# Kernel tuning notes

Hardware: AMD Instinct MI355X
Metric: run time of the kernel (lower is better)

## Reference

```python
import math
import jax, jax.numpy as jnp
import numpy as np

N = 20000
E = 640000
H = 256          # hidden_channels
HEADS = 8
HD = H // HEADS  # head_dim = 32
RBF = 64
CUT = 5.0
EPS = 1e-5


def setup_inputs() -> dict:
    key = jax.random.key(0)
    ks = jax.random.split(key, 24)
    g = lambda k, shape, scale: (jax.random.normal(k, shape, dtype=jnp.float32) * scale)
    inp = {
        "x": jax.random.normal(ks[0], (N, H), dtype=jnp.float32),
        "vec": jax.random.normal(ks[1], (N, 3, H), dtype=jnp.float32),
        "edge_index": jax.random.randint(ks[2], (2, E), 0, N),
        "r_ij": jax.random.uniform(ks[3], (E,), dtype=jnp.float32) * CUT,
        "f_ij": jax.random.normal(ks[4], (E, RBF), dtype=jnp.float32),
        "d_ij": jax.random.normal(ks[5], (E, 3), dtype=jnp.float32),
        # parameters (weights stored as [in, out], applied as x @ W + b)
        "ln_w": jnp.ones((H,), jnp.float32),
        "ln_b": jnp.zeros((H,), jnp.float32),
        "Wq": g(ks[6], (H, H), 1.0 / math.sqrt(H)),
        "bq": jnp.zeros((H,), jnp.float32),
        "Wk": g(ks[7], (H, H), 1.0 / math.sqrt(H)),
        "bk": jnp.zeros((H,), jnp.float32),
        "Wv": g(ks[8], (H, 3 * H), 1.0 / math.sqrt(H)),
        "bv": jnp.zeros((3 * H,), jnp.float32),
        "Wo": g(ks[9], (H, 3 * H), 1.0 / math.sqrt(H)),
        "bo": jnp.zeros((3 * H,), jnp.float32),
        "Wvec": g(ks[10], (H, 3 * H), 1.0 / math.sqrt(H)),  # no bias
        "Wdk": g(ks[11], (RBF, H), 1.0 / math.sqrt(RBF)),
        "bdk": jnp.zeros((H,), jnp.float32),
        "Wdv": g(ks[12], (RBF, 3 * H), 1.0 / math.sqrt(RBF)),
        "bdv": jnp.zeros((3 * H,), jnp.float32),
    }
    return inp


def reference(x, vec, edge_index, r_ij, f_ij, d_ij,
              ln_w, ln_b, Wq, bq, Wk, bk, Wv, bv, Wo, bo,
              Wvec, Wdk, bdk, Wdv, bdv):
    silu = jax.nn.silu
    n = x.shape[0]

    # LayerNorm over hidden dim
    mu = x.mean(-1, keepdims=True)
    var = ((x - mu) ** 2).mean(-1, keepdims=True)
    xn = (x - mu) / jnp.sqrt(var + EPS) * ln_w + ln_b

    q = (xn @ Wq + bq).reshape(n, HEADS, HD)
    k = (xn @ Wk + bk).reshape(n, HEADS, HD)
    v = (xn @ Wv + bv).reshape(n, HEADS, 3 * HD)

    # vec_proj: [N,3,H] @ [H,3H] -> split into three [N,3,H]
    vec1, vec2, vec3 = jnp.split(vec @ Wvec, 3, axis=-1)
    vec_dot = (vec1 * vec2).sum(axis=1)              # [N, H]
    vec_h = vec.reshape(n, 3, HEADS, HD)

    dk = silu(f_ij @ Wdk + bdk).reshape(-1, HEADS, HD)        # [E,h,hd]
    dv = silu(f_ij @ Wdv + bdv).reshape(-1, HEADS, 3 * HD)    # [E,h,3hd]

    src = edge_index[0]  # j (source)
    dst = edge_index[1]  # i (target), aggregation index

    # per-edge attention with cosine cutoff (cutoff_lower = 0)
    attn = (q[dst] * k[src] * dk).sum(-1)                      # [E, h]
    cut = 0.5 * (jnp.cos(r_ij * (math.pi / CUT)) + 1.0)
    cut = cut * (r_ij < CUT).astype(cut.dtype)
    attn = silu(attn) * cut[:, None]

    v_j = v[src] * dv                                          # [E,h,3hd]
    xm, v1m, v2m = jnp.split(v_j, 3, axis=2)                   # each [E,h,hd]
    xm = xm * attn[..., None]                                  # [E,h,hd]
    # [E,3,h,hd]
    vecm = vec_h[src] * v1m[:, None] + v2m[:, None] * d_ij[:, :, None, None]

    x_agg = jax.ops.segment_sum(xm, dst, num_segments=n).reshape(n, H)
    vec_agg = jax.ops.segment_sum(vecm, dst, num_segments=n).reshape(n, 3, H)

    o1, o2, o3 = jnp.split(x_agg @ Wo + bo, 3, axis=1)
    dx = vec_dot * o2 + o3
    dvec = vec3 * o1[:, None] + vec_agg
    return dx, dvec
```

## Files before the change

### kernel.cpp

```cpp
#include <hip/hip_runtime.h>

#define NN 20000
#define EE 640000
#define H 256
#define H3 768

typedef __attribute__((ext_vector_type(8))) short bfrag;
typedef __attribute__((ext_vector_type(4))) float f32x4;
typedef __attribute__((ext_vector_type(2))) unsigned short u16x2;
typedef __attribute__((ext_vector_type(4))) unsigned short u16x4;
typedef unsigned short u16;

__device__ __forceinline__ float silu_f(float x){ return x / (1.f + __expf(-x)); }

__device__ __forceinline__ u16 f2bf(float f){
  union { float fv; unsigned u; } a; a.fv = f;
  unsigned r = a.u + 0x7fffu + ((a.u >> 16) & 1u);
  return (u16)(r >> 16);
}
__device__ __forceinline__ float bf2f(u16 u){
  union { unsigned u32; float f; } a; a.u32 = ((unsigned)u) << 16; return a.f;
}

__global__ __launch_bounds__(256) void ln_kernel(
    const float* __restrict__ x, const float* __restrict__ w,
    const float* __restrict__ b, float* __restrict__ xn)
{
  int n = blockIdx.x, t = threadIdx.x;
  float v = x[(size_t)n*H + t];
  float s1 = v, s2 = v*v;
  #pragma unroll
  for(int o=32;o>0;o>>=1){ s1 += __shfl_down(s1,o,64); s2 += __shfl_down(s2,o,64); }
  __shared__ float r1[4], r2[4];
  if((t&63)==0){ r1[t>>6]=s1; r2[t>>6]=s2; }
  __syncthreads();
  float mu  = (r1[0]+r1[1]+r1[2]+r1[3]) * (1.f/256.f);
  float ex2 = (r2[0]+r2[1]+r2[2]+r2[3]) * (1.f/256.f);
  float inv = rsqrtf(ex2 - mu*mu + 1e-5f);
  xn[(size_t)n*H + t] = (v - mu)*inv*w[t] + b[t];
}

template<int MODE>
__global__ __launch_bounds__(256) void gemm_node(
    const float* __restrict__ A, const float* __restrict__ W, int ldw,
    const float* __restrict__ bias, float* __restrict__ C,
    u16* __restrict__ Ch, long bufstride, int M)
{
  __shared__ float As[16][68];
  __shared__ float Bs[16][64];
  int tid = threadIdx.x;
  int m0 = blockIdx.x * 64;
  int n0 = blockIdx.y * 64;
  int tx = tid & 15, ty = tid >> 4;
  int arow = tid >> 2;
  int ak   = (tid & 3) * 4;
  int brow = tid >> 4;
  int bcol = (tid & 15) * 4;
  bool aval = (m0 + arow) < M;
  const float* Ap = A + (size_t)(m0 + arow) * 256;
  float acc[4][4] = {};
  for(int kb = 0; kb < 256; kb += 16){
    float4 av = make_float4(0.f,0.f,0.f,0.f);
    if(aval) av = *(const float4*)(Ap + kb + ak);
    As[ak+0][arow] = av.x; As[ak+1][arow] = av.y;
    As[ak+2][arow] = av.z; As[ak+3][arow] = av.w;
    *(float4*)&Bs[brow][bcol] = *(const float4*)(W + (size_t)(kb + brow)*ldw + n0 + bcol);
    __syncthreads();
    #pragma unroll
    for(int kk=0;kk<16;kk++){
      float4 a4 = *(const float4*)&As[kk][ty*4];
      float4 b4 = *(const float4*)&Bs[kk][tx*4];
      float aa[4] = {a4.x,a4.y,a4.z,a4.w};
      float bb[4] = {b4.x,b4.y,b4.z,b4.w};
      #pragma unroll
      for(int i=0;i<4;i++)
        #pragma unroll
        for(int j=0;j<4;j++)
          acc[i][j] += aa[i]*bb[j];
    }
    __syncthreads();
  }
  #pragma unroll
  for(int i=0;i<4;i++){
    int row = m0 + ty*4 + i;
    if(row < M){
      int col = n0 + tx*4;
      float o[4];
      #pragma unroll
      for(int j=0;j<4;j++) o[j] = acc[i][j] + (bias ? bias[col+j] : 0.f);
      if(MODE == 0){
        *(float4*)(C + (size_t)row*ldw + col) = make_float4(o[0],o[1],o[2],o[3]);
      } else if(MODE == 1){
        u16x4 h; h[0]=f2bf(o[0]); h[1]=f2bf(o[1]); h[2]=f2bf(o[2]); h[3]=f2bf(o[3]);
        *(u16x4*)(Ch + (size_t)row*ldw + col) = h;
      } else {
        int buf = n0 >> 8;
        int coff = (n0 & 255) + tx*4;
        *(float4*)(C + (size_t)buf*bufstride + (size_t)row*256 + coff)
            = make_float4(o[0],o[1],o[2],o[3]);
      }
    }
  }
}

__global__ __launch_bounds__(256) void vecdot_kernel(
    const float* __restrict__ vp1, const float* __restrict__ vp2, float* __restrict__ vd)
{
  int i = blockIdx.x*256 + threadIdx.x;
  int n = i >> 8, c = i & 255;
  size_t base = (size_t)(3*n)*256 + c;
  float s = 0.f;
  #pragma unroll
  for(int d=0;d<3;d++) s += vp1[base + d*256] * vp2[base + d*256];
  vd[i] = s;
}

__global__ __launch_bounds__(256) void cvt_bf16(
    const float* __restrict__ src, u16* __restrict__ dst, int n4)
{
  int i = blockIdx.x*256 + threadIdx.x;
  if(i < n4){
    float4 v = ((const float4*)src)[i];
    u16x4 o; o[0]=f2bf(v.x); o[1]=f2bf(v.y); o[2]=f2bf(v.z); o[3]=f2bf(v.w);
    ((u16x4*)dst)[i] = o;
  }
}

__global__ __launch_bounds__(256) void hist_kernel(const int* __restrict__ ei, int* __restrict__ deg){
  int e = blockIdx.x*256 + threadIdx.x;
  if(e < EE) atomicAdd(&deg[ei[EE + e]], 1);
}

__global__ __launch_bounds__(1024) void scan_kernel(const int* __restrict__ deg, int* __restrict__ offs){
  __shared__ int ps[1024];
  int t = threadIdx.x;
  int base = t*20;
  int s = 0;
  for(int i=0;i<20;i++){ int idx = base+i; if(idx < NN) s += deg[idx]; }
  ps[t] = s; __syncthreads();
  for(int off=1; off<1024; off<<=1){
    int v = (t>=off) ? ps[t-off] : 0;
    __syncthreads();
    ps[t] += v;
    __syncthreads();
  }
  int run = (t==0) ? 0 : ps[t-1];
  for(int i=0;i<20;i++){
    int idx = base+i;
    if(idx <= NN){
      offs[idx] = run;
      if(idx < NN) run += deg[idx];
    }
  }
}

__global__ __launch_bounds__(256) void scatter_kernel(
    const int* __restrict__ ei, const int* __restrict__ offs,
    int* __restrict__ cursor, int* __restrict__ perm)
{
  int e = blockIdx.x*256 + threadIdx.x;
  if(e >= EE) return;
  int d = ei[EE + e];
  int r = atomicAdd(&cursor[d], 1);
  perm[offs[d] + r] = e;
}

__global__ __launch_bounds__(256) void conv_wdk(const float* __restrict__ Wdk, short* __restrict__ wdkf){
  int idx = blockIdx.x*256 + threadIdx.x;
  int k = idx >> 8, c = idx & 255;
  int g = c >> 6, rem = c & 63, n15 = rem >> 2, p = rem & 3;
  int half = k >> 5, quad = (k >> 3) & 3, j = k & 7;
  wdkf[(g*4+p)*1024 + half*512 + quad*128 + n15*8 + j] = (short)f2bf(Wdk[k*H + c]);
}

__global__ __launch_bounds__(256) void conv_wdv(const float* __restrict__ Wdv, short* __restrict__ wdvf){
  int idx = blockIdx.x*256 + threadIdx.x;
  int k = idx / 768, c = idx % 768;
  int h = c / 96, jj = c % 96;
  int st = jj >> 5, r32 = jj & 31, n15 = r32 >> 1, p = r32 & 1;
  int sub = h*6 + st*2 + p;
  int half = k >> 5, quad = (k >> 3) & 3, j = k & 7;
  wdvf[sub*1024 + half*512 + quad*128 + n15*8 + j] = (short)f2bf(Wdv[k*H3 + c]);
}

__global__ __launch_bounds__(256,3) void edge_kernel(
    const int* __restrict__ ei, const float* __restrict__ rij,
    const float* __restrict__ fij, const float* __restrict__ dij,
    const float* __restrict__ qg, const u16* __restrict__ kh,
    const u16* __restrict__ vh, const u16* __restrict__ vech,
    const short* __restrict__ wdkf, const short* __restrict__ wdvf,
    const float* __restrict__ bdk, const float* __restrict__ bdv,
    const int* __restrict__ offs, const int* __restrict__ perm,
    float* __restrict__ xagg, float* __restrict__ dvec)
{
  __shared__ float accs_x[4][256];
  __shared__ float accs_v[4][768];
  __shared__ float attn_s[4][16][8];
  __shared__ int   esrc_s[4][16];
  __shared__ float ecut_s[4][16];
  __shared__ float emask_s[4][16];
  __shared__ float edij_s[4][3][16];

  int tid  = threadIdx.x;
  int wv   = tid >> 6, lane = tid & 63;
  int ln15 = lane & 15, quad = lane >> 4;
  int n    = blockIdx.x*4 + wv;
  int rs = offs[n], re = offs[n+1];

  #pragma unroll
  for(int i=0;i<4;i++)  accs_x[wv][i*64 + lane] = 0.f;
  #pragma unroll
  for(int i=0;i<12;i++) accs_v[wv][i*64 + lane] = 0.f;

  float qreg[16], bkreg[16];
  #pragma unroll
  for(int g=0; g<4; g++){
    float4 t = *(const float4*)(qg + (size_t)n*H + g*64 + 4*ln15);
    qreg[g*4+0]=t.x; qreg[g*4+1]=t.y; qreg[g*4+2]=t.z; qreg[g*4+3]=t.w;
    float4 u = *(const float4*)(bdk + g*64 + 4*ln15);
    bkreg[g*4+0]=u.x; bkreg[g*4+1]=u.y; bkreg[g*4+2]=u.z; bkreg[g*4+3]=u.w;
  }

  for(int base = rs; base < re; base += 16){
    int idx = base + ln15;
    bool val = idx < re;
    int e = perm[val ? idx : rs];
    if(quad == 0){
      esrc_s[wv][ln15] = ei[e];
      float r = rij[e];
      float cu = 0.5f*(__cosf(r*0.6283185307f)+1.f);
      cu = (r < 5.f) ? cu : 0.f;
      ecut_s[wv][ln15]  = val ? cu : 0.f;
      emask_s[wv][ln15] = val ? 1.f : 0.f;
      edij_s[wv][0][ln15] = dij[e*3+0];
      edij_s[wv][1][ln15] = dij[e*3+1];
      edij_s[wv][2][ln15] = dij[e*3+2];
    }
    bfrag af0, af1;
    {
      const float* fr = fij + (size_t)e*64 + quad*8;
      float4 fa = *(const float4*)fr;
      float4 fb = *(const float4*)(fr+4);
      float4 fc = *(const float4*)(fr+32);
      float4 fd = *(const float4*)(fr+36);
      af0[0]=(short)f2bf(fa.x); af0[1]=(short)f2bf(fa.y); af0[2]=(short)f2bf(fa.z); af0[3]=(short)f2bf(fa.w);
      af0[4]=(short)f2bf(fb.x); af0[5]=(short)f2bf(fb.y); af0[6]=(short)f2bf(fb.z); af0[7]=(short)f2bf(fb.w);
      af1[0]=(short)f2bf(fc.x); af1[1]=(short)f2bf(fc.y); af1[2]=(short)f2bf(fc.z); af1[3]=(short)f2bf(fc.w);
      af1[4]=(short)f2bf(fd.x); af1[5]=(short)f2bf(fd.y); af1[6]=(short)f2bf(fd.z); af1[7]=(short)f2bf(fd.w);
    }
    int sns[4]; float mk[4];
    #pragma unroll
    for(int r=0;r<4;r++){
      int el = quad*4 + r;
      sns[r] = esrc_s[wv][el];
      mk[r]  = emask_s[wv][el];
    }

    u16x4 kr[4][4];
    #pragma unroll
    for(int g=0;g<4;g++)
      #pragma unroll
      for(int r=0;r<4;r++)
        kr[g][r] = *(const u16x4*)(kh + (size_t)sns[r]*H + g*64 + 4*ln15);

    #pragma unroll
    for(int g=0;g<4;g++){
      float lgg[4] = {0.f,0.f,0.f,0.f};
      #pragma unroll
      for(int p=0;p<4;p++){
        const short* wp = wdkf + (g*4+p)*1024 + quad*128 + ln15*8;
        bfrag b0 = *(const bfrag*)wp;
        bfrag b1 = *(const bfrag*)(wp + 512);
        f32x4 acc = {0.f,0.f,0.f,0.f};
        acc = __builtin_amdgcn_mfma_f32_16x16x32_bf16(af0, b0, acc, 0,0,0);
        acc = __builtin_amdgcn_mfma_f32_16x16x32_bf16(af1, b1, acc, 0,0,0);
        float bias = bkreg[g*4+p], qv = qreg[g*4+p];
        #pragma unroll
        for(int r=0;r<4;r++){
          float dk = silu_f(acc[r] + bias);
          lgg[r] += dk * qv * bf2f(kr[g][r][p]);
        }
      }
      #pragma unroll
      for(int r=0;r<4;r++){
        lgg[r] += __shfl_xor(lgg[r],1,64);
        lgg[r] += __shfl_xor(lgg[r],2,64);
        lgg[r] += __shfl_xor(lgg[r],4,64);
      }
      if((ln15 & 7) == 0){
        int hh = 2*g + (ln15 >> 3);
        #pragma unroll
        for(int r=0;r<4;r++){
          int el = quad*4 + r;
          attn_s[wv][el][hh] = silu_f(lgg[r]) * ecut_s[wv][el];
        }
      }
    }

    #pragma unroll 1
    for(int h=0;h<8;h++){
      u16x2 vld[3][4], vcl[3][4];
      #pragma unroll
      for(int st=0;st<3;st++)
        #pragma unroll
        for(int r=0;r<4;r++)
          vld[st][r] = *(const u16x2*)(vh + (size_t)sns[r]*H3 + h*96 + st*32 + 2*ln15);
      #pragma unroll
      for(int d=0;d<3;d++)
        #pragma unroll
        for(int r=0;r<4;r++)
          vcl[d][r] = *(const u16x2*)(vech + (size_t)sns[r]*H3 + d*H + h*32 + 2*ln15);
      float bb[6];
      #pragma unroll
      for(int st=0;st<3;st++){
        float2 b2 = *(const float2*)(bdv + h*96 + st*32 + 2*ln15);
        bb[st*2] = b2.x; bb[st*2+1] = b2.y;
      }
      float at[4];
      #pragma unroll
      for(int r=0;r<4;r++) at[r] = attn_s[wv][quad*4+r][h];

      float v1v[2][4], vjv[2][4];
      float xmt[2] = {0.f, 0.f};
      #pragma unroll
      for(int st=0;st<3;st++){
        #pragma unroll
        for(int p=0;p<2;p++){
          const short* wp = wdvf + (h*6+st*2+p)*1024 + quad*128 + ln15*8;
          bfrag b0 = *(const bfrag*)wp;
          bfrag b1 = *(const bfrag*)(wp + 512);
          f32x4 acc = {0.f,0.f,0.f,0.f};
          acc = __builtin_amdgcn_mfma_f32_16x16x32_bf16(af0, b0, acc, 0,0,0);
          acc = __builtin_amdgcn_mfma_f32_16x16x32_bf16(af1, b1, acc, 0,0,0);
          float bias = bb[st*2+p];
          #pragma unroll
          for(int r=0;r<4;r++){
            float dvv = silu_f(acc[r] + bias) * mk[r];
            float vj = bf2f(vld[st][r][p]) * dvv;
            if(st == 0)      xmt[p]    += vj * at[r];
            else if(st == 1) v1v[p][r]  = vj;
            else             vjv[p][r]  = vj;
          }
        }
      }
      #pragma unroll
      for(int p=0;p<2;p++){
        xmt[p] += __shfl_xor(xmt[p],16,64);
        xmt[p] += __shfl_xor(xmt[p],32,64);
      }
      if(quad == 0){
        accs_x[wv][h*32 + 2*ln15 + 0] += xmt[0];
        accs_x[wv][h*32 + 2*ln15 + 1] += xmt[1];
      }
      #pragma unroll
      for(int d=0;d<3;d++){
        float t0 = 0.f, t1 = 0.f;
        #pragma unroll
        for(int r=0;r<4;r++){
          float dj = edij_s[wv][d][quad*4+r];
          t0 += bf2f(vcl[d][r][0]) * v1v[0][r] + dj * vjv[0][r];
          t1 += bf2f(vcl[d][r][1]) * v1v[1][r] + dj * vjv[1][r];
        }
        t0 += __shfl_xor(t0,16,64); t0 += __shfl_xor(t0,32,64);
        t1 += __shfl_xor(t1,16,64); t1 += __shfl_xor(t1,32,64);
        if(quad == 0){
          accs_v[wv][d*H + h*32 + 2*ln15 + 0] += t0;
          accs_v[wv][d*H + h*32 + 2*ln15 + 1] += t1;
        }
      }
    }
  }

  #pragma unroll
  for(int j=0;j<4;j++)  xagg[(size_t)n*H  + j*64 + lane] = accs_x[wv][j*64 + lane];
  #pragma unroll
  for(int j=0;j<12;j++) dvec[(size_t)n*H3 + j*64 + lane] = accs_v[wv][j*64 + lane];
}

__global__ __launch_bounds__(256) void final_kernel(
    const float* __restrict__ ob, const float* __restrict__ vd,
    const float* __restrict__ vp3, float* __restrict__ out)
{
  int i = blockIdx.x*256 + threadIdx.x;
  int n = i >> 8, c = i & 255;
  float o1 = ob[(size_t)n*H3 + c];
  float o2 = ob[(size_t)n*H3 + 256 + c];
  float o3 = ob[(size_t)n*H3 + 512 + c];
  out[i] = vd[i]*o2 + o3;
  float* dvec = out + (size_t)NN*H;
  #pragma unroll
  for(int d=0;d<3;d++){
    dvec[(size_t)n*H3 + d*H + c] += vp3[(size_t)(3*n+d)*256 + c] * o1;
  }
}

extern "C" void kernel_launch(void* const* d_in, const int* in_sizes, int n_in,
                              void* d_out, int out_size, void* d_ws, size_t ws_size,
                              hipStream_t stream){
  (void)in_sizes; (void)n_in; (void)out_size; (void)ws_size;
  const float* x    = (const float*)d_in[0];
  const float* vec  = (const float*)d_in[1];
  const int*   ei   = (const int*)d_in[2];
  const float* rij  = (const float*)d_in[3];
  const float* fij  = (const float*)d_in[4];
  const float* dij  = (const float*)d_in[5];
  const float* ln_w = (const float*)d_in[6];
  const float* ln_b = (const float*)d_in[7];
  const float* Wq   = (const float*)d_in[8];
  const float* bq   = (const float*)d_in[9];
  const float* Wk   = (const float*)d_in[10];
  const float* bk   = (const float*)d_in[11];
  const float* Wv   = (const float*)d_in[12];
  const float* bv   = (const float*)d_in[13];
  const float* Wo   = (const float*)d_in[14];
  const float* bo   = (const float*)d_in[15];
  const float* Wvec = (const float*)d_in[16];
  const float* Wdk  = (const float*)d_in[17];
  const float* bdk  = (const float*)d_in[18];
  const float* Wdv  = (const float*)d_in[19];
  const float* bdv  = (const float*)d_in[20];
  float* out = (float*)d_out;
  float* ws  = (float*)d_ws;

  float* qb   = ws;
  float* vd   = ws +  5120000;
  float* xagg = ws + 10240000;
  float* vp1  = ws + 15360000;
  float* vp2  = ws + 30720000;
  float* vp3  = ws + 46080000;
  u16*   kh   = (u16*)(ws + 61440000);
  u16*   vh   = (u16*)(ws + 64000000);
  u16*   vech = (u16*)(ws + 71680000);
  int* deg    = (int*)(ws + 79360000);
  int* offs   = deg + 20032;
  int* cursor = offs + 20032;
  int* perm   = cursor + 20032;
  short* wdkf = (short*)(perm + 640000);
  short* wdvf = wdkf + 16384;

  float* xn = vp1;
  float* ob = vp1;
  float* dvec = out + (size_t)NN*H;

  ln_kernel<<<20000, 256, 0, stream>>>(x, ln_w, ln_b, xn);
  gemm_node<0><<<dim3(313,4),  256, 0, stream>>>(xn, Wq, 256, bq, qb, nullptr, 0, 20000);
  gemm_node<1><<<dim3(313,4),  256, 0, stream>>>(xn, Wk, 256, bk, nullptr, kh, 0, 20000);
  gemm_node<1><<<dim3(313,12), 256, 0, stream>>>(xn, Wv, 768, bv, nullptr, vh, 0, 20000);

  hipMemsetAsync(deg,    0, 20000*sizeof(int), stream);
  hipMemsetAsync(cursor, 0, 20000*sizeof(int), stream);
  hist_kernel<<<2500, 256, 0, stream>>>(ei, deg);
  scan_kernel<<<1, 1024, 0, stream>>>(deg, offs);
  scatter_kernel<<<2500, 256, 0, stream>>>(ei, offs, cursor, perm);
  conv_wdk<<<64,  256, 0, stream>>>(Wdk, wdkf);
  conv_wdv<<<192, 256, 0, stream>>>(Wdv, wdvf);
  cvt_bf16<<<15000, 256, 0, stream>>>(vec, vech, 3840000);

  gemm_node<2><<<dim3(938,12), 256, 0, stream>>>(vec, Wvec, 768, nullptr, vp1, nullptr, 15360000L, 60000);
  vecdot_kernel<<<20000, 256, 0, stream>>>(vp1, vp2, vd);

  edge_kernel<<<5000, 256, 0, stream>>>(ei, rij, fij, dij, qb, kh, vh, vech,
                                        wdkf, wdvf, bdk, bdv, offs, perm,
                                        xagg, dvec);

  gemm_node<0><<<dim3(313,12), 256, 0, stream>>>(xagg, Wo, 768, bo, ob, nullptr, 0, 20000);
  final_kernel<<<20000, 256, 0, stream>>>(ob, vd, vp3, out);
}
```

Before: 2.365 ms.

## Replace FP32 SIMT node GEMMs with split-bf16 MFMA GEMMs and fuse vecdot

Moves all node-level GEMMs (Q/K/V, vec projection, output projection) from scalar FP32 tiled loops onto bf16 MFMA instructions. Near-FP32 accuracy is kept by splitting each operand into hi/lo bf16 parts and issuing three MFMAs per tile. Weights are transposed and split once per call, and layernorm, the vec conversion and the edge aggregation now write hi/lo bf16 outputs directly. The vec1·vec2 product is fused into the projection GEMM through LDS, so the vp1/vp2 intermediates are never written to memory. In exchange it uses three MFMAs per tile and extra conversion kernels, and the GEMMs load fragments straight from global memory with no LDS staging.

```diff
diff --git a/kernel.cpp b/kernel.cpp
--- a/kernel.cpp
+++ b/kernel.cpp
@@ -24,7 +24,7 @@
 
 __global__ __launch_bounds__(256) void ln_kernel(
     const float* __restrict__ x, const float* __restrict__ w,
-    const float* __restrict__ b, float* __restrict__ xn)
+    const float* __restrict__ b, u16* __restrict__ xnh, u16* __restrict__ xnl)
 {
   int n = blockIdx.x, t = threadIdx.x;
   float v = x[(size_t)n*H + t];
@@ -37,92 +37,186 @@
   float mu  = (r1[0]+r1[1]+r1[2]+r1[3]) * (1.f/256.f);
   float ex2 = (r2[0]+r2[1]+r2[2]+r2[3]) * (1.f/256.f);
   float inv = rsqrtf(ex2 - mu*mu + 1e-5f);
-  xn[(size_t)n*H + t] = (v - mu)*inv*w[t] + b[t];
-}
-
-template<int MODE>
-__global__ __launch_bounds__(256) void gemm_node(
-    const float* __restrict__ A, const float* __restrict__ W, int ldw,
-    const float* __restrict__ bias, float* __restrict__ C,
-    u16* __restrict__ Ch, long bufstride, int M)
-{
-  __shared__ float As[16][68];
-  __shared__ float Bs[16][64];
-  int tid = threadIdx.x;
-  int m0 = blockIdx.x * 64;
-  int n0 = blockIdx.y * 64;
-  int tx = tid & 15, ty = tid >> 4;
-  int arow = tid >> 2;
-  int ak   = (tid & 3) * 4;
-  int brow = tid >> 4;
-  int bcol = (tid & 15) * 4;
-  bool aval = (m0 + arow) < M;
-  const float* Ap = A + (size_t)(m0 + arow) * 256;
-  float acc[4][4] = {};
-  for(int kb = 0; kb < 256; kb += 16){
-    float4 av = make_float4(0.f,0.f,0.f,0.f);
-    if(aval) av = *(const float4*)(Ap + kb + ak);
-    As[ak+0][arow] = av.x; As[ak+1][arow] = av.y;
-    As[ak+2][arow] = av.z; As[ak+3][arow] = av.w;
-    *(float4*)&Bs[brow][bcol] = *(const float4*)(W + (size_t)(kb + brow)*ldw + n0 + bcol);
-    __syncthreads();
-    #pragma unroll
-    for(int kk=0;kk<16;kk++){
-      float4 a4 = *(const float4*)&As[kk][ty*4];
-      float4 b4 = *(const float4*)&Bs[kk][tx*4];
-      float aa[4] = {a4.x,a4.y,a4.z,a4.w};
-      float bb[4] = {b4.x,b4.y,b4.z,b4.w};
-      #pragma unroll
-      for(int i=0;i<4;i++)
-        #pragma unroll
-        for(int j=0;j<4;j++)
-          acc[i][j] += aa[i]*bb[j];
-    }
-    __syncthreads();
-  }
-  #pragma unroll
-  for(int i=0;i<4;i++){
-    int row = m0 + ty*4 + i;
-    if(row < M){
-      int col = n0 + tx*4;
-      float o[4];
-      #pragma unroll
-      for(int j=0;j<4;j++) o[j] = acc[i][j] + (bias ? bias[col+j] : 0.f);
-      if(MODE == 0){
-        *(float4*)(C + (size_t)row*ldw + col) = make_float4(o[0],o[1],o[2],o[3]);
-      } else if(MODE == 1){
-        u16x4 h; h[0]=f2bf(o[0]); h[1]=f2bf(o[1]); h[2]=f2bf(o[2]); h[3]=f2bf(o[3]);
-        *(u16x4*)(Ch + (size_t)row*ldw + col) = h;
-      } else {
-        int buf = n0 >> 8;
-        int coff = (n0 & 255) + tx*4;
-        *(float4*)(C + (size_t)buf*bufstride + (size_t)row*256 + coff)
-            = make_float4(o[0],o[1],o[2],o[3]);
-      }
-    }
-  }
-}
-
-__global__ __launch_bounds__(256) void vecdot_kernel(
-    const float* __restrict__ vp1, const float* __restrict__ vp2, float* __restrict__ vd)
-{
-  int i = blockIdx.x*256 + threadIdx.x;
-  int n = i >> 8, c = i & 255;
-  size_t base = (size_t)(3*n)*256 + c;
-  float s = 0.f;
-  #pragma unroll
-  for(int d=0;d<3;d++) s += vp1[base + d*256] * vp2[base + d*256];
-  vd[i] = s;
-}
-
-__global__ __launch_bounds__(256) void cvt_bf16(
-    const float* __restrict__ src, u16* __restrict__ dst, int n4)
+  float y = (v - mu)*inv*w[t] + b[t];
+  u16 h = f2bf(y);
+  xnh[(size_t)n*H + t] = h;
+  xnl[(size_t)n*H + t] = f2bf(y - bf2f(h));
+}
+
+__global__ __launch_bounds__(256) void wconv(
+    const float* __restrict__ W, int ldw,
+    u16* __restrict__ oh, u16* __restrict__ ol, int mode)
+{
+  int idx = blockIdx.x*256 + threadIdx.x;
+  int n = idx >> 8, k = idx & 255;
+  int c = n;
+  if(mode == 1){
+    int y = n >> 7, j = n & 127;
+    c = (j < 64) ? (y*64 + j) : (256 + y*64 + (j - 64));
+  }
+  float f = W[(size_t)k*ldw + c];
+  u16 h = f2bf(f);
+  oh[idx] = h;
+  ol[idx] = f2bf(f - bf2f(h));
+}
+
+__global__ __launch_bounds__(256) void cvt_vec(
+    const float* __restrict__ src, u16* __restrict__ hi, u16* __restrict__ lo, int n4)
 {
   int i = blockIdx.x*256 + threadIdx.x;
   if(i < n4){
     float4 v = ((const float4*)src)[i];
-    u16x4 o; o[0]=f2bf(v.x); o[1]=f2bf(v.y); o[2]=f2bf(v.z); o[3]=f2bf(v.w);
-    ((u16x4*)dst)[i] = o;
+    u16x4 oh, olo;
+    float a[4] = {v.x, v.y, v.z, v.w};
+    #pragma unroll
+    for(int j=0;j<4;j++){
+      u16 h = f2bf(a[j]);
+      oh[j]  = h;
+      olo[j] = f2bf(a[j] - bf2f(h));
+    }
+    ((u16x4*)hi)[i] = oh;
+    ((u16x4*)lo)[i] = olo;
+  }
+}
+
+template<int OUT>
+__global__ __launch_bounds__(256) void gemm_split(
+    const u16* __restrict__ Ah, const u16* __restrict__ Al,
+    const u16* __restrict__ Bh, const u16* __restrict__ Bl,
+    const float* __restrict__ bias,
+    float* __restrict__ Cf, u16* __restrict__ Ch, int ldw, int M)
+{
+  int tid  = threadIdx.x;
+  int wid  = tid >> 6, lane = tid & 63;
+  int ln15 = lane & 15, quad = lane >> 4;
+  int wr = wid >> 1, wc = wid & 1;
+  int m0 = blockIdx.x*128 + wr*64;
+  int n0 = blockIdx.y*128 + wc*64;
+
+  int arow[4];
+  #pragma unroll
+  for(int mi=0;mi<4;mi++){
+    int r = m0 + mi*16 + ln15;
+    arow[mi] = (r < M) ? r : (M-1);
+  }
+  int ncol[4];
+  #pragma unroll
+  for(int ni=0;ni<4;ni++) ncol[ni] = n0 + ni*16 + ln15;
+
+  f32x4 acc[4][4] = {};
+
+  #pragma unroll 2
+  for(int ks=0; ks<8; ks++){
+    int kb = ks*32 + quad*8;
+    bfrag ah[4], al[4], bh[4], bl[4];
+    #pragma unroll
+    for(int mi=0;mi<4;mi++){
+      ah[mi] = *(const bfrag*)(Ah + ((size_t)arow[mi] << 8) + kb);
+      al[mi] = *(const bfrag*)(Al + ((size_t)arow[mi] << 8) + kb);
+    }
+    #pragma unroll
+    for(int ni=0;ni<4;ni++){
+      bh[ni] = *(const bfrag*)(Bh + ((size_t)ncol[ni] << 8) + kb);
+      bl[ni] = *(const bfrag*)(Bl + ((size_t)ncol[ni] << 8) + kb);
+    }
+    #pragma unroll
+    for(int mi=0;mi<4;mi++)
+      #pragma unroll
+      for(int ni=0;ni<4;ni++){
+        acc[mi][ni] = __builtin_amdgcn_mfma_f32_16x16x32_bf16(ah[mi], bh[ni], acc[mi][ni], 0,0,0);
+        acc[mi][ni] = __builtin_amdgcn_mfma_f32_16x16x32_bf16(ah[mi], bl[ni], acc[mi][ni], 0,0,0);
+        acc[mi][ni] = __builtin_amdgcn_mfma_f32_16x16x32_bf16(al[mi], bh[ni], acc[mi][ni], 0,0,0);
+      }
+  }
+
+  #pragma unroll
+  for(int mi=0;mi<4;mi++){
+    #pragma unroll
+    for(int ni=0;ni<4;ni++){
+      int col = ncol[ni];
+      float bs = bias ? bias[col] : 0.f;
+      #pragma unroll
+      for(int r=0;r<4;r++){
+        int row = m0 + mi*16 + quad*4 + r;
+        if(row < M){
+          float v = acc[mi][ni][r] + bs;
+          if(OUT == 0) Cf[(size_t)row*ldw + col] = v;
+          else         Ch[(size_t)row*ldw + col] = f2bf(v);
+        }
+      }
+    }
+  }
+}
+
+__global__ __launch_bounds__(256) void gemm_vecdot(
+    const u16* __restrict__ Ah, const u16* __restrict__ Al,
+    const u16* __restrict__ Bh, const u16* __restrict__ Bl,
+    float* __restrict__ vd)
+{
+  __shared__ float l1[96][66];
+  __shared__ float l2[96][66];
+  int tid  = threadIdx.x;
+  int wid  = tid >> 6, lane = tid & 63;
+  int ln15 = lane & 15, quad = lane >> 4;
+  int wr = wid >> 1, wc = wid & 1;
+  int m0 = blockIdx.x*96;
+  int y  = blockIdx.y;
+  int rowb = wr*48;
+
+  int arow[3];
+  #pragma unroll
+  for(int mi=0;mi<3;mi++) arow[mi] = m0 + rowb + mi*16 + ln15;
+  int ncol[4];
+  #pragma unroll
+  for(int ni=0;ni<4;ni++) ncol[ni] = y*128 + wc*64 + ni*16 + ln15;
+
+  f32x4 acc[3][4] = {};
+
+  #pragma unroll 2
+  for(int ks=0; ks<8; ks++){
+    int kb = ks*32 + quad*8;
+    bfrag ah[3], al[3], bh[4], bl[4];
+    #pragma unroll
+    for(int mi=0;mi<3;mi++){
+      ah[mi] = *(const bfrag*)(Ah + ((size_t)arow[mi] << 8) + kb);
+      al[mi] = *(const bfrag*)(Al + ((size_t)arow[mi] << 8) + kb);
+    }
+    #pragma unroll
+    for(int ni=0;ni<4;ni++){
+      bh[ni] = *(const bfrag*)(Bh + ((size_t)ncol[ni] << 8) + kb);
+      bl[ni] = *(const bfrag*)(Bl + ((size_t)ncol[ni] << 8) + kb);
+    }
+    #pragma unroll
+    for(int mi=0;mi<3;mi++)
+      #pragma unroll
+      for(int ni=0;ni<4;ni++){
+        acc[mi][ni] = __builtin_amdgcn_mfma_f32_16x16x32_bf16(ah[mi], bh[ni], acc[mi][ni], 0,0,0);
+        acc[mi][ni] = __builtin_amdgcn_mfma_f32_16x16x32_bf16(ah[mi], bl[ni], acc[mi][ni], 0,0,0);
+        acc[mi][ni] = __builtin_amdgcn_mfma_f32_16x16x32_bf16(al[mi], bh[ni], acc[mi][ni], 0,0,0);
+      }
+  }
+
+  #pragma unroll
+  for(int mi=0;mi<3;mi++)
+    #pragma unroll
+    for(int ni=0;ni<4;ni++)
+      #pragma unroll
+      for(int r=0;r<4;r++){
+        int lr = rowb + mi*16 + quad*4 + r;
+        int lc = ni*16 + ln15;
+        if(wc == 0) l1[lr][lc] = acc[mi][ni][r];
+        else        l2[lr][lc] = acc[mi][ni][r];
+      }
+  __syncthreads();
+
+  #pragma unroll
+  for(int i=0;i<8;i++){
+    int id  = i*256 + tid;
+    int n_l = id >> 6, c = id & 63;
+    float s = 0.f;
+    #pragma unroll
+    for(int d=0;d<3;d++) s += l1[n_l*3+d][c] * l2[n_l*3+d][c];
+    vd[((size_t)(blockIdx.x*32 + n_l) << 8) + y*64 + c] = s;
   }
 }
 
@@ -191,7 +285,7 @@
     const short* __restrict__ wdkf, const short* __restrict__ wdvf,
     const float* __restrict__ bdk, const float* __restrict__ bdv,
     const int* __restrict__ offs, const int* __restrict__ perm,
-    float* __restrict__ xagg, float* __restrict__ dvec)
+    u16* __restrict__ xaggh, u16* __restrict__ xaggl, float* __restrict__ dvec)
 {
   __shared__ float accs_x[4][256];
   __shared__ float accs_v[4][768];
@@ -372,7 +466,12 @@
   }
 
   #pragma unroll
-  for(int j=0;j<4;j++)  xagg[(size_t)n*H  + j*64 + lane] = accs_x[wv][j*64 + lane];
+  for(int j=0;j<4;j++){
+    float v = accs_x[wv][j*64 + lane];
+    u16 h = f2bf(v);
+    xaggh[(size_t)n*H + j*64 + lane] = h;
+    xaggl[(size_t)n*H + j*64 + lane] = f2bf(v - bf2f(h));
+  }
   #pragma unroll
   for(int j=0;j<12;j++) dvec[(size_t)n*H3 + j*64 + lane] = accs_v[wv][j*64 + lane];
 }
@@ -422,30 +521,51 @@
   float* out = (float*)d_out;
   float* ws  = (float*)d_ws;
 
-  float* qb   = ws;
-  float* vd   = ws +  5120000;
-  float* xagg = ws + 10240000;
-  float* vp1  = ws + 15360000;
-  float* vp2  = ws + 30720000;
-  float* vp3  = ws + 46080000;
-  u16*   kh   = (u16*)(ws + 61440000);
-  u16*   vh   = (u16*)(ws + 64000000);
-  u16*   vech = (u16*)(ws + 71680000);
-  int* deg    = (int*)(ws + 79360000);
-  int* offs   = deg + 20032;
-  int* cursor = offs + 20032;
-  int* perm   = cursor + 20032;
-  short* wdkf = (short*)(perm + 640000);
-  short* wdvf = wdkf + 16384;
-
-  float* xn = vp1;
-  float* ob = vp1;
+  float* vd    = ws;
+  float* ob    = ws +  5120000;
+  float* vp3   = ws + 20480000;
+  float* qb    = ws + 35840000;
+  u16*   kh    = (u16*)(ws + 40960000);
+  u16*   vh    = (u16*)(ws + 43520000);
+  u16*   vech  = (u16*)(ws + 51200000);
+  u16*   vecl  = (u16*)(ws + 58880000);
+  u16*   xnh   = (u16*)(ws + 66560000);
+  u16*   xnl   = (u16*)(ws + 69120000);
+  u16*   xaggh = (u16*)(ws + 71680000);
+  u16*   xaggl = (u16*)(ws + 74240000);
+  u16*   wt    = (u16*)(ws + 76800000);
+  int*   deg    = (int*)(ws + 77530000);
+  int*   offs   = deg + 20032;
+  int*   cursor = offs + 20032;
+  int*   perm   = cursor + 20032;
+  short* wdkf   = (short*)(perm + 640000);
+  short* wdvf   = wdkf + 16384;
+
+  u16* wtq_h = wt;            u16* wtq_l = wt +   65536;
+  u16* wtk_h = wt +  131072;  u16* wtk_l = wt +  196608;
+  u16* wtv_h = wt +  262144;  u16* wtv_l = wt +  458752;
+  u16* wto_h = wt +  655360;  u16* wto_l = wt +  851968;
+  u16* wtp_h = wt + 1048576;  u16* wtp_l = wt + 1179648;
+  u16* wt3_h = wt + 1310720;  u16* wt3_l = wt + 1376256;
+
   float* dvec = out + (size_t)NN*H;
 
-  ln_kernel<<<20000, 256, 0, stream>>>(x, ln_w, ln_b, xn);
-  gemm_node<0><<<dim3(313,4),  256, 0, stream>>>(xn, Wq, 256, bq, qb, nullptr, 0, 20000);
-  gemm_node<1><<<dim3(313,4),  256, 0, stream>>>(xn, Wk, 256, bk, nullptr, kh, 0, 20000);
-  gemm_node<1><<<dim3(313,12), 256, 0, stream>>>(xn, Wv, 768, bv, nullptr, vh, 0, 20000);
+  ln_kernel<<<20000, 256, 0, stream>>>(x, ln_w, ln_b, xnh, xnl);
+
+  wconv<<<256, 256, 0, stream>>>(Wq,        256, wtq_h, wtq_l, 0);
+  wconv<<<256, 256, 0, stream>>>(Wk,        256, wtk_h, wtk_l, 0);
+  wconv<<<768, 256, 0, stream>>>(Wv,        768, wtv_h, wtv_l, 0);
+  wconv<<<768, 256, 0, stream>>>(Wo,        768, wto_h, wto_l, 0);
+  wconv<<<512, 256, 0, stream>>>(Wvec,      768, wtp_h, wtp_l, 1);
+  wconv<<<256, 256, 0, stream>>>(Wvec + 512,768, wt3_h, wt3_l, 0);
+
+  gemm_split<0><<<dim3(157,2), 256, 0, stream>>>(xnh, xnl, wtq_h, wtq_l, bq, qb, nullptr, 256, 20000);
+  gemm_split<1><<<dim3(157,2), 256, 0, stream>>>(xnh, xnl, wtk_h, wtk_l, bk, nullptr, kh, 256, 20000);
+  gemm_split<1><<<dim3(157,6), 256, 0, stream>>>(xnh, xnl, wtv_h, wtv_l, bv, nullptr, vh, 768, 20000);
+
+  cvt_vec<<<15000, 256, 0, stream>>>(vec, vech, vecl, 3840000);
+  gemm_vecdot<<<dim3(625,4), 256, 0, stream>>>(vech, vecl, wtp_h, wtp_l, vd);
+  gemm_split<0><<<dim3(469,2), 256, 0, stream>>>(vech, vecl, wt3_h, wt3_l, nullptr, vp3, nullptr, 256, 60000);
 
   hipMemsetAsync(deg,    0, 20000*sizeof(int), stream);
   hipMemsetAsync(cursor, 0, 20000*sizeof(int), stream);
@@ -454,15 +574,11 @@
   scatter_kernel<<<2500, 256, 0, stream>>>(ei, offs, cursor, perm);
   conv_wdk<<<64,  256, 0, stream>>>(Wdk, wdkf);
   conv_wdv<<<192, 256, 0, stream>>>(Wdv, wdvf);
-  cvt_bf16<<<15000, 256, 0, stream>>>(vec, vech, 3840000);
-
-  gemm_node<2><<<dim3(938,12), 256, 0, stream>>>(vec, Wvec, 768, nullptr, vp1, nullptr, 15360000L, 60000);
-  vecdot_kernel<<<20000, 256, 0, stream>>>(vp1, vp2, vd);
 
   edge_kernel<<<5000, 256, 0, stream>>>(ei, rij, fij, dij, qb, kh, vh, vech,
                                         wdkf, wdvf, bdk, bdv, offs, perm,
-                                        xagg, dvec);
-
-  gemm_node<0><<<dim3(313,12), 256, 0, stream>>>(xagg, Wo, 768, bo, ob, nullptr, 0, 20000);
+                                        xaggh, xaggl, dvec);
+
+  gemm_split<0><<<dim3(157,6), 256, 0, stream>>>(xaggh, xaggl, wto_h, wto_l, bo, ob, nullptr, 768, 20000);
   final_kernel<<<20000, 256, 0, stream>>>(ob, vd, vp3, out);
 }
```

After: 2.100 ms. 1.13x faster.
